# Kernel tuning notes

Measured on AMD Instinct MI355X. Metric: run time of the kernel, lower is better.

## Reference

```python
import jax, jax.numpy as jnp
import numpy as np

B, MN, GN, ME, GE = 1, 40962, 65160, 327660, 163848
MEMB = EEMB = 256
H1, H2 = 512, 64
EPS = 1e-5


def setup_inputs() -> dict:
    key = jax.random.key(0)
    ks = jax.random.split(key, 16)
    s = 0.05
    return {
        "gx": jax.random.normal(ks[0], (B, GN, MEMB), jnp.float32),
        "mx": jax.random.normal(ks[1], (B, MN, MEMB), jnp.float32),
        "me_i": jax.random.randint(ks[2], (2, ME), 0, MN),
        "me_x": jax.random.normal(ks[3], (B, ME, EEMB), jnp.float32),
        "g2me_i": jax.random.randint(ks[4], (2, GE), 0, MN),
        "g2me_x": jax.random.normal(ks[5], (B, GE, EEMB), jnp.float32),
        "m2ge_i": jax.random.randint(ks[6], (2, GE), 0, MN),
        "m2ge_x": jax.random.normal(ks[7], (B, GE, EEMB), jnp.float32),
        # learned params (Linear stored as [in, out]; y = x @ W + b, math-equivalent to torch)
        "W1": jax.random.normal(ks[8], (2 * MEMB + EEMB, H1), jnp.float32) * s,
        "b1": jnp.zeros((H1,), jnp.float32),
        "W2": jax.random.normal(ks[9], (H1, H2), jnp.float32) * s,
        "b2": jnp.zeros((H2,), jnp.float32),
        "W3": jax.random.normal(ks[10], (H2, EEMB), jnp.float32) * s,
        "b3": jnp.zeros((EEMB,), jnp.float32),
        # LayerNorm([m_enum, eemb]) -> elementwise affine over last two dims
        "ln_w": jnp.ones((ME, EEMB), jnp.float32),
        "ln_b": jnp.zeros((ME, EEMB), jnp.float32),
    }


def reference(gx, mx, me_i, me_x, g2me_i, g2me_x, m2ge_i, m2ge_x,
              W1, b1, W2, b2, W3, b3, ln_w, ln_b):
    row, col = me_i[0], me_i[1]
    # gather sender/receiver mesh-node features per edge: [B, ME, 2*MEMB+EEMB]
    h = jnp.concatenate([mx[:, row], mx[:, col], me_x], axis=-1)
    h = jax.nn.silu(h @ W1 + b1)
    h = jax.nn.silu(h @ W2 + b2)
    h = h @ W3 + b3
    # LayerNorm over the last TWO dims (m_enum, eemb), as nn.LayerNorm([m_enum, eemb])
    mean = jnp.mean(h, axis=(-2, -1), keepdims=True)
    var = jnp.var(h, axis=(-2, -1), keepdims=True)
    h = (h - mean) * jax.lax.rsqrt(var + EPS) * ln_w + ln_b
    me_x_new = me_x + h
    return (gx, mx, me_i, me_x_new, g2me_i, g2me_x, m2ge_i, m2ge_x)
```

## Files before the change

### kernel.cpp

```cpp
#include <hip/hip_runtime.h>
#include <hip/hip_bf16.h>

typedef unsigned short u16;
typedef unsigned int u32;
typedef __attribute__((ext_vector_type(8))) short bfrag8;
typedef __attribute__((ext_vector_type(4))) float f32x4;

#define ME_N 327660
#define MN_N 40962
#define MEMB_N 256
#define H1_N 512
#define H2_N 64
#define EEMB_N 256
#define LN_EPS 1e-5f
#define NBLK 5120

static __device__ __forceinline__ u16 f2bf(float f) {
  __hip_bfloat16 h = __float2bfloat16(f);
  return *reinterpret_cast<u16*>(&h);
}
static __device__ __forceinline__ float bf2f(u16 u) {
  union { u32 i; float f; } x; x.i = ((u32)u) << 16; return x.f;
}
static __device__ __forceinline__ u32 pack2(float a, float b) {
  return (u32)f2bf(a) | ((u32)f2bf(b) << 16);
}
static __device__ __forceinline__ float silu_f(float x) {
  return x / (1.0f + __expf(-x));
}
static __device__ __forceinline__ void gload_lds16(const void* g, void* l) {
  __builtin_amdgcn_global_load_lds(
      (const __attribute__((address_space(1))) void*)g,
      (__attribute__((address_space(3))) void*)l, 16, 0, 0);
}

__global__ void i2f_kernel(const int* __restrict__ src, float* __restrict__ dst, int n) {
  int i = blockIdx.x * 256 + threadIdx.x;
  if (i < n) dst[i] = (float)src[i];
}

__global__ void bfconv_kernel(const float* __restrict__ src, u16* __restrict__ dst, int n) {
  int i = (blockIdx.x * 256 + threadIdx.x) * 8;
  if (i >= n) return;
  float4 v0 = reinterpret_cast<const float4*>(src + i)[0];
  float4 v1 = reinterpret_cast<const float4*>(src + i)[1];
  uint4 q;
  q.x = pack2(v0.x, v0.y); q.y = pack2(v0.z, v0.w);
  q.z = pack2(v1.x, v1.y); q.w = pack2(v1.z, v1.w);
  *reinterpret_cast<uint4*>(dst + i) = q;
}

__global__ void wconv1_kernel(const float* __restrict__ src, u16* __restrict__ dst) {
  int i = blockIdx.x * 256 + threadIdx.x;
  if (i >= 512 * 768) return;
  int e   = i & 7;
  int l16 = (i >> 3) & 15;
  int k4  = (i >> 7) & 3;
  int ks  = (i >> 9) & 1;
  int rest = i >> 10;
  int kc = rest % 12;
  int J  = rest / 12;
  int n = J * 16 + l16;
  int k = kc * 64 + ks * 32 + k4 * 8 + e;
  dst[i] = f2bf(src[(size_t)k * 512 + n]);
}

__global__ void wconv_kernel(const float* __restrict__ src, u16* __restrict__ dst,
                             int K, int N) {
  int i = blockIdx.x * 256 + threadIdx.x;
  if (i >= K * N) return;
  int n = i / K;
  int k = i - n * K;
  dst[i] = f2bf(src[(size_t)k * N + n]);
}

__launch_bounds__(256, 2)
__global__ void gemm_fused_kernel(const u16* __restrict__ mxb, const int* __restrict__ me_i,
                                  const float* __restrict__ me_x,
                                  const u16* __restrict__ w1f, const float* __restrict__ b1,
                                  const u16* __restrict__ w2t, const float* __restrict__ b2,
                                  const u16* __restrict__ w3t, const float* __restrict__ b3,
                                  u16* __restrict__ h3, float* __restrict__ partials) {
  __shared__ u16 S[64 * 520 + 64 * 72];
  __shared__ float red[8];
  u16* Abuf = S;
  u16* h1T  = S;
  u16* h2T  = S + 64 * 520;

  const int t = threadIdx.x;
  const int m0 = blockIdx.x * 64;
  const int lane = t & 63;
  const int wid = t >> 6;
  const int l16 = lane & 15;
  const int k4 = lane >> 4;

  const int c0 = wid * 128 + lane;
  const int c1 = c0 + 64;
  const int r0 = c0 >> 3, r1 = c1 >> 3;
  const int e0s = ((c0 & 7) ^ (r0 & 7)) * 8;
  const int e1s = ((c1 & 7) ^ (r1 & 7)) * 8;
  const int mg0 = min(m0 + r0, ME_N - 1);
  const int mg1 = min(m0 + r1, ME_N - 1);
  const u16* row0r = mxb + (size_t)me_i[mg0] * MEMB_N;
  const u16* row0c = mxb + (size_t)me_i[ME_N + mg0] * MEMB_N;
  const u16* row1r = mxb + (size_t)me_i[mg1] * MEMB_N;
  const u16* row1c = mxb + (size_t)me_i[ME_N + mg1] * MEMB_N;
  const int rr = t >> 2, g = t & 3;
  const float* pe = me_x + (size_t)min(m0 + rr, ME_N - 1) * EEMB_N;
  const int E0 = (g * 16) ^ ((rr & 7) * 8);
  const int E1 = (g * 16 + 8) ^ ((rr & 7) * 8);

  const f32x4 zero = {0.f, 0.f, 0.f, 0.f};
  f32x4 acc[4][8];
#pragma unroll
  for (int i = 0; i < 4; ++i)
#pragma unroll
    for (int j = 0; j < 8; ++j) acc[i][j] = zero;

  auto stage_A = [&](int kcn) {
    if (kcn < 8) {
      const u16* s0 = (kcn < 4 ? row0r : row0c) + ((kcn & 3) * 64 + e0s);
      const u16* s1 = (kcn < 4 ? row1r : row1c) + ((kcn & 3) * 64 + e1s);
      u16* lb = Abuf + (kcn & 1) * 4096 + wid * 1024;
      gload_lds16(s0, lb);
      gload_lds16(s1, lb + 512);
    } else {
      const float4* p4 = reinterpret_cast<const float4*>(pe + (kcn - 8) * 64 + g * 16);
      float4 v0 = p4[0], v1 = p4[1], v2 = p4[2], v3 = p4[3];
      uint4 qa, qb;
      qa.x = pack2(v0.x, v0.y); qa.y = pack2(v0.z, v0.w);
      qa.z = pack2(v1.x, v1.y); qa.w = pack2(v1.z, v1.w);
      qb.x = pack2(v2.x, v2.y); qb.y = pack2(v2.z, v2.w);
      qb.z = pack2(v3.x, v3.y); qb.w = pack2(v3.z, v3.w);
      u16* d = Abuf + (kcn & 1) * 4096 + rr * 64;
      *reinterpret_cast<uint4*>(d + E0) = qa;
      *reinterpret_cast<uint4*>(d + E1) = qb;
    }
  };

  stage_A(0);
  __syncthreads();

  for (int kc = 0; kc < 12; ++kc) {
    if (kc < 11) stage_A(kc + 1);
    bfrag8 bfr[2][8];
    {
      const u16* bb = w1f + (size_t)kc * 1024 + k4 * 128 + l16 * 8;
      const size_t woff = (size_t)(wid * 8) * 12288;
#pragma unroll
      for (int ks = 0; ks < 2; ++ks)
#pragma unroll
        for (int j = 0; j < 8; ++j)
          bfr[ks][j] = *reinterpret_cast<const bfrag8*>(bb + woff + (size_t)j * 12288 + ks * 512);
    }
    const u16* ab = Abuf + (kc & 1) * 4096;
#pragma unroll
    for (int ks = 0; ks < 2; ++ks) {
      bfrag8 a[4];
#pragma unroll
      for (int i = 0; i < 4; ++i)
        a[i] = *reinterpret_cast<const bfrag8*>(
            &ab[(i * 16 + l16) * 64 + ((ks * 32 + k4 * 8) ^ ((l16 & 7) * 8))]);
#pragma unroll
      for (int i = 0; i < 4; ++i)
#pragma unroll
        for (int j = 0; j < 8; ++j)
          acc[i][j] = __builtin_amdgcn_mfma_f32_16x16x32_bf16(a[i], bfr[ks][j], acc[i][j], 0, 0, 0);
    }
    __syncthreads();
  }

  float b1v[8];
#pragma unroll
  for (int j = 0; j < 8; ++j) b1v[j] = b1[wid * 128 + j * 16 + l16];
#pragma unroll
  for (int i = 0; i < 4; ++i)
#pragma unroll
    for (int j = 0; j < 8; ++j)
#pragma unroll
      for (int rg = 0; rg < 4; ++rg) {
        float v = silu_f(acc[i][j][rg] + b1v[j]);
        h1T[(i * 16 + k4 * 4 + rg) * 520 + wid * 128 + j * 16 + l16] = f2bf(v);
      }
  __syncthreads();

  const int n2 = wid * 16 + l16;
  bfrag8 w2f[16];
#pragma unroll
  for (int ks = 0; ks < 16; ++ks)
    w2f[ks] = *reinterpret_cast<const bfrag8*>(w2t + (size_t)n2 * 512 + ks * 32 + k4 * 8);
  f32x4 acc2[4];
#pragma unroll
  for (int i = 0; i < 4; ++i) acc2[i] = zero;
#pragma unroll
  for (int ks = 0; ks < 16; ++ks) {
#pragma unroll
    for (int i = 0; i < 4; ++i) {
      bfrag8 a2 = *reinterpret_cast<const bfrag8*>(&h1T[(i * 16 + l16) * 520 + ks * 32 + k4 * 8]);
      acc2[i] = __builtin_amdgcn_mfma_f32_16x16x32_bf16(a2, w2f[ks], acc2[i], 0, 0, 0);
    }
  }
  const float b2v = b2[n2];
#pragma unroll
  for (int i = 0; i < 4; ++i)
#pragma unroll
    for (int rg = 0; rg < 4; ++rg) {
      float v = silu_f(acc2[i][rg] + b2v);
      h2T[(i * 16 + k4 * 4 + rg) * 72 + n2] = f2bf(v);
    }
  __syncthreads();

  bfrag8 w3f[4][2];
#pragma unroll
  for (int j = 0; j < 4; ++j)
#pragma unroll
    for (int ks = 0; ks < 2; ++ks)
      w3f[j][ks] = *reinterpret_cast<const bfrag8*>(
          w3t + (size_t)(wid * 64 + j * 16 + l16) * 64 + ks * 32 + k4 * 8);
  f32x4 acc3[4][4];
#pragma unroll
  for (int i = 0; i < 4; ++i)
#pragma unroll
    for (int j = 0; j < 4; ++j) acc3[i][j] = zero;
#pragma unroll
  for (int ks = 0; ks < 2; ++ks) {
    bfrag8 a3[4];
#pragma unroll
    for (int i = 0; i < 4; ++i)
      a3[i] = *reinterpret_cast<const bfrag8*>(&h2T[(i * 16 + l16) * 72 + ks * 32 + k4 * 8]);
#pragma unroll
    for (int i = 0; i < 4; ++i)
#pragma unroll
      for (int j = 0; j < 4; ++j)
        acc3[i][j] = __builtin_amdgcn_mfma_f32_16x16x32_bf16(a3[i], w3f[j][ks], acc3[i][j], 0, 0, 0);
  }

  float b3v[4];
#pragma unroll
  for (int j = 0; j < 4; ++j) b3v[j] = b3[wid * 64 + j * 16 + l16];
  float lsum = 0.f, lsq = 0.f;
#pragma unroll
  for (int i = 0; i < 4; ++i)
#pragma unroll
    for (int rg = 0; rg < 4; ++rg) {
      int m = m0 + i * 16 + k4 * 4 + rg;
      if (m < ME_N) {
#pragma unroll
        for (int j = 0; j < 4; ++j) {
          float v = acc3[i][j][rg] + b3v[j];
          h3[(size_t)m * EEMB_N + wid * 64 + j * 16 + l16] = f2bf(v);
          lsum += v;
          lsq += v * v;
        }
      }
    }
#pragma unroll
  for (int o = 32; o > 0; o >>= 1) {
    lsum += __shfl_down(lsum, o, 64);
    lsq  += __shfl_down(lsq, o, 64);
  }
  if (lane == 0) { red[wid] = lsum; red[4 + wid] = lsq; }
  __syncthreads();
  if (t == 0) {
    partials[2 * blockIdx.x]     = red[0] + red[1] + red[2] + red[3];
    partials[2 * blockIdx.x + 1] = red[4] + red[5] + red[6] + red[7];
  }
}

__global__ void reduce_kernel(const float* __restrict__ partials, int n,
                              float* __restrict__ stats) {
  __shared__ float s1[256], s2[256];
  float a = 0.f, b = 0.f;
  for (int i = threadIdx.x; i < n; i += 256) { a += partials[2 * i]; b += partials[2 * i + 1]; }
  s1[threadIdx.x] = a; s2[threadIdx.x] = b;
  __syncthreads();
  for (int off = 128; off > 0; off >>= 1) {
    if ((int)threadIdx.x < off) {
      s1[threadIdx.x] += s1[threadIdx.x + off];
      s2[threadIdx.x] += s2[threadIdx.x + off];
    }
    __syncthreads();
  }
  if (threadIdx.x == 0) {
    double cnt = (double)ME_N * (double)EEMB_N;
    double mean = (double)s1[0] / cnt;
    double var = (double)s2[0] / cnt - mean * mean;
    stats[0] = (float)mean;
    stats[1] = (float)(1.0 / sqrt(var + (double)LN_EPS));
  }
}

__launch_bounds__(256)
__global__ void final_kernel(const u16* __restrict__ h3, const float* __restrict__ me_x,
                             const float* __restrict__ ln_w, const float* __restrict__ ln_b,
                             const float* __restrict__ stats, float* __restrict__ out) {
  const size_t total = (size_t)ME_N * EEMB_N;
  size_t i = ((size_t)blockIdx.x * 256 + threadIdx.x) * 8;
  if (i >= total) return;
  const float mean = stats[0], inv = stats[1];
  uint4 hv = *reinterpret_cast<const uint4*>(h3 + i);
  float h[8];
  h[0] = bf2f((u16)(hv.x & 0xffff)); h[1] = bf2f((u16)(hv.x >> 16));
  h[2] = bf2f((u16)(hv.y & 0xffff)); h[3] = bf2f((u16)(hv.y >> 16));
  h[4] = bf2f((u16)(hv.z & 0xffff)); h[5] = bf2f((u16)(hv.z >> 16));
  h[6] = bf2f((u16)(hv.w & 0xffff)); h[7] = bf2f((u16)(hv.w >> 16));
  float4 m0 = reinterpret_cast<const float4*>(me_x + i)[0];
  float4 m1 = reinterpret_cast<const float4*>(me_x + i)[1];
  float4 w0 = reinterpret_cast<const float4*>(ln_w + i)[0];
  float4 w1 = reinterpret_cast<const float4*>(ln_w + i)[1];
  float4 c0 = reinterpret_cast<const float4*>(ln_b + i)[0];
  float4 c1 = reinterpret_cast<const float4*>(ln_b + i)[1];
  float4 o0, o1;
  o0.x = m0.x + (h[0] - mean) * inv * w0.x + c0.x;
  o0.y = m0.y + (h[1] - mean) * inv * w0.y + c0.y;
  o0.z = m0.z + (h[2] - mean) * inv * w0.z + c0.z;
  o0.w = m0.w + (h[3] - mean) * inv * w0.w + c0.w;
  o1.x = m1.x + (h[4] - mean) * inv * w1.x + c1.x;
  o1.y = m1.y + (h[5] - mean) * inv * w1.y + c1.y;
  o1.z = m1.z + (h[6] - mean) * inv * w1.z + c1.z;
  o1.w = m1.w + (h[7] - mean) * inv * w1.w + c1.w;
  reinterpret_cast<float4*>(out + i)[0] = o0;
  reinterpret_cast<float4*>(out + i)[1] = o1;
}

extern "C" void kernel_launch(void* const* d_in, const int* in_sizes, int n_in,
                              void* d_out, int out_size, void* d_ws, size_t ws_size,
                              hipStream_t stream) {
  const float* mx   = (const float*)d_in[1];
  const int*   me_i = (const int*)d_in[2];
  const float* me_x = (const float*)d_in[3];
  const float* W1 = (const float*)d_in[8];
  const float* b1 = (const float*)d_in[9];
  const float* W2 = (const float*)d_in[10];
  const float* b2 = (const float*)d_in[11];
  const float* W3 = (const float*)d_in[12];
  const float* b3 = (const float*)d_in[13];
  const float* ln_w = (const float*)d_in[14];
  const float* ln_b = (const float*)d_in[15];

  char* ws = (char*)d_ws;
  u16* w1f = (u16*)(ws + 0);
  u16* w2t = (u16*)(ws + 786432);
  u16* w3t = (u16*)(ws + 851968);
  u16* mxb = (u16*)(ws + 884736);
  u16* h3  = (u16*)(ws + 21857280);
  float* partials = (float*)(ws + 189619200);
  float* stats    = (float*)(ws + 189660160);

  size_t off[8]; size_t a = 0;
  for (int i = 0; i < 8; ++i) { off[i] = a; a += (size_t)in_sizes[i]; }

  for (int i = 0; i < 8; ++i) {
    if (i == 3) continue;
    if (i == 2 || i == 4 || i == 6) {
      int n = in_sizes[i];
      i2f_kernel<<<(n + 255) / 256, 256, 0, stream>>>(
          (const int*)d_in[i], (float*)d_out + off[i], n);
    } else {
      hipMemcpyAsync((char*)d_out + off[i] * 4, d_in[i], (size_t)in_sizes[i] * 4,
                     hipMemcpyDeviceToDevice, stream);
    }
  }

  wconv1_kernel<<<(512 * 768 + 255) / 256, 256, 0, stream>>>(W1, w1f);
  wconv_kernel<<<(512 * 64 + 255) / 256, 256, 0, stream>>>(W2, w2t, 512, 64);
  wconv_kernel<<<(64 * 256 + 255) / 256, 256, 0, stream>>>(W3, w3t, 64, 256);
  {
    int n = MN_N * MEMB_N;
    bfconv_kernel<<<(n / 8 + 255) / 256, 256, 0, stream>>>(mx, mxb, n);
  }

  gemm_fused_kernel<<<NBLK, 256, 0, stream>>>(mxb, me_i, me_x, w1f, b1, w2t, b2,
                                              w3t, b3, h3, partials);
  reduce_kernel<<<1, 256, 0, stream>>>(partials, NBLK, stats);

  const size_t total8 = (size_t)ME_N * EEMB_N / 8;
  final_kernel<<<(int)((total8 + 255) / 256), 256, 0, stream>>>(
      h3, me_x, ln_w, ln_b, stats, (float*)d_out + off[3]);
}
```

Measured before the change: 911.8 us.

## Rework fused MLP kernel to 8 waves with smaller LDS and coalesced output

Moves the fused edge-MLP kernel from 4 to 8 waves per 64-row block and shrinks shared memory from about 75KB to 32KB, so more blocks and waves can be resident per CU. Layer 1 switches MFMA operand order, so each wave holds a 16-row by 64-column slice of the output instead of 32 registers' worth of accumulator tiles. Layer 2 is split-K across wave halves, with each half computing its own h1 half and the partial sums reduced through LDS. Layer 3 results are staged in swizzled LDS and written to h3 as coalesced 16-byte rows; the workspace offsets shift so the padded last block can write past the real row count. This adds extra barriers and an LDS reduction step, and lowers the per-thread register budget, which risks spills.

```diff
diff --git a/kernel.cpp b/kernel.cpp
--- a/kernel.cpp
+++ b/kernel.cpp
@@ -74,67 +74,51 @@
   dst[i] = f2bf(src[(size_t)k * N + n]);
 }
 
-__launch_bounds__(256, 2)
+__launch_bounds__(512, 4)
 __global__ void gemm_fused_kernel(const u16* __restrict__ mxb, const int* __restrict__ me_i,
                                   const float* __restrict__ me_x,
                                   const u16* __restrict__ w1f, const float* __restrict__ b1,
                                   const u16* __restrict__ w2t, const float* __restrict__ b2,
                                   const u16* __restrict__ w3t, const float* __restrict__ b3,
                                   u16* __restrict__ h3, float* __restrict__ partials) {
-  __shared__ u16 S[64 * 520 + 64 * 72];
-  __shared__ float red[8];
-  u16* Abuf = S;
-  u16* h1T  = S;
-  u16* h2T  = S + 64 * 520;
+  __shared__ u16 S[16384];
+  __shared__ float red[16];
 
   const int t = threadIdx.x;
   const int m0 = blockIdx.x * 64;
   const int lane = t & 63;
-  const int wid = t >> 6;
+  const int w = t >> 6;
   const int l16 = lane & 15;
   const int k4 = lane >> 4;
-
-  const int c0 = wid * 128 + lane;
-  const int c1 = c0 + 64;
-  const int r0 = c0 >> 3, r1 = c1 >> 3;
-  const int e0s = ((c0 & 7) ^ (r0 & 7)) * 8;
-  const int e1s = ((c1 & 7) ^ (r1 & 7)) * 8;
-  const int mg0 = min(m0 + r0, ME_N - 1);
-  const int mg1 = min(m0 + r1, ME_N - 1);
-  const u16* row0r = mxb + (size_t)me_i[mg0] * MEMB_N;
-  const u16* row0c = mxb + (size_t)me_i[ME_N + mg0] * MEMB_N;
-  const u16* row1r = mxb + (size_t)me_i[mg1] * MEMB_N;
-  const u16* row1c = mxb + (size_t)me_i[ME_N + mg1] * MEMB_N;
-  const int rr = t >> 2, g = t & 3;
-  const float* pe = me_x + (size_t)min(m0 + rr, ME_N - 1) * EEMB_N;
-  const int E0 = (g * 16) ^ ((rr & 7) * 8);
-  const int E1 = (g * 16 + 8) ^ ((rr & 7) * 8);
+  const int h7 = l16 & 7;
+
+  const int r_st = t >> 3;
+  const int g_st = t & 7;
+  const int gsw = ((g_st ^ (r_st & 7)) * 8);
+  const int mg = min(m0 + r_st, ME_N - 1);
+  const u16* rowr = mxb + (size_t)me_i[mg] * MEMB_N;
+  const u16* rowc = mxb + (size_t)me_i[ME_N + mg] * MEMB_N;
+  const float* pe = me_x + (size_t)mg * EEMB_N;
 
   const f32x4 zero = {0.f, 0.f, 0.f, 0.f};
-  f32x4 acc[4][8];
-#pragma unroll
-  for (int i = 0; i < 4; ++i)
-#pragma unroll
-    for (int j = 0; j < 8; ++j) acc[i][j] = zero;
+  f32x4 acc[4][4];
+#pragma unroll
+  for (int jj = 0; jj < 4; ++jj)
+#pragma unroll
+    for (int i = 0; i < 4; ++i) acc[jj][i] = zero;
 
   auto stage_A = [&](int kcn) {
+    const int buf = (kcn & 1) * 4096;
     if (kcn < 8) {
-      const u16* s0 = (kcn < 4 ? row0r : row0c) + ((kcn & 3) * 64 + e0s);
-      const u16* s1 = (kcn < 4 ? row1r : row1c) + ((kcn & 3) * 64 + e1s);
-      u16* lb = Abuf + (kcn & 1) * 4096 + wid * 1024;
-      gload_lds16(s0, lb);
-      gload_lds16(s1, lb + 512);
+      const u16* src = (kcn < 4 ? rowr : rowc) + (kcn & 3) * 64 + gsw;
+      gload_lds16(src, S + buf + w * 512);
     } else {
-      const float4* p4 = reinterpret_cast<const float4*>(pe + (kcn - 8) * 64 + g * 16);
-      float4 v0 = p4[0], v1 = p4[1], v2 = p4[2], v3 = p4[3];
-      uint4 qa, qb;
-      qa.x = pack2(v0.x, v0.y); qa.y = pack2(v0.z, v0.w);
-      qa.z = pack2(v1.x, v1.y); qa.w = pack2(v1.z, v1.w);
-      qb.x = pack2(v2.x, v2.y); qb.y = pack2(v2.z, v2.w);
-      qb.z = pack2(v3.x, v3.y); qb.w = pack2(v3.z, v3.w);
-      u16* d = Abuf + (kcn & 1) * 4096 + rr * 64;
-      *reinterpret_cast<uint4*>(d + E0) = qa;
-      *reinterpret_cast<uint4*>(d + E1) = qb;
+      const float4* p4 = reinterpret_cast<const float4*>(pe + (kcn - 8) * 64 + g_st * 8);
+      float4 v0 = p4[0], v1 = p4[1];
+      uint4 q;
+      q.x = pack2(v0.x, v0.y); q.y = pack2(v0.z, v0.w);
+      q.z = pack2(v1.x, v1.y); q.w = pack2(v1.z, v1.w);
+      *reinterpret_cast<uint4*>(S + buf + r_st * 64 + gsw) = q;
     }
   };
 
@@ -143,127 +127,169 @@
 
   for (int kc = 0; kc < 12; ++kc) {
     if (kc < 11) stage_A(kc + 1);
-    bfrag8 bfr[2][8];
-    {
-      const u16* bb = w1f + (size_t)kc * 1024 + k4 * 128 + l16 * 8;
-      const size_t woff = (size_t)(wid * 8) * 12288;
-#pragma unroll
-      for (int ks = 0; ks < 2; ++ks)
-#pragma unroll
-        for (int j = 0; j < 8; ++j)
-          bfr[ks][j] = *reinterpret_cast<const bfrag8*>(bb + woff + (size_t)j * 12288 + ks * 512);
-    }
-    const u16* ab = Abuf + (kc & 1) * 4096;
+    const u16* ab = S + (kc & 1) * 4096;
+    const u16* wb = w1f + (size_t)w * 12288 + (size_t)kc * 1024 + k4 * 128 + l16 * 8;
 #pragma unroll
     for (int ks = 0; ks < 2; ++ks) {
       bfrag8 a[4];
 #pragma unroll
       for (int i = 0; i < 4; ++i)
         a[i] = *reinterpret_cast<const bfrag8*>(
-            &ab[(i * 16 + l16) * 64 + ((ks * 32 + k4 * 8) ^ ((l16 & 7) * 8))]);
-#pragma unroll
-      for (int i = 0; i < 4; ++i)
-#pragma unroll
-        for (int j = 0; j < 8; ++j)
-          acc[i][j] = __builtin_amdgcn_mfma_f32_16x16x32_bf16(a[i], bfr[ks][j], acc[i][j], 0, 0, 0);
+            &ab[(i * 16 + l16) * 64 + (((ks * 4 + k4) ^ h7) * 8)]);
+#pragma unroll
+      for (int jj = 0; jj < 4; ++jj) {
+        bfrag8 bf = *reinterpret_cast<const bfrag8*>(wb + (size_t)jj * 98304 + ks * 512);
+#pragma unroll
+        for (int i = 0; i < 4; ++i)
+          acc[jj][i] = __builtin_amdgcn_mfma_f32_16x16x32_bf16(bf, a[i], acc[jj][i], 0, 0, 0);
+      }
     }
     __syncthreads();
   }
 
-  float b1v[8];
-#pragma unroll
-  for (int j = 0; j < 8; ++j) b1v[j] = b1[wid * 128 + j * 16 + l16];
-#pragma unroll
-  for (int i = 0; i < 4; ++i)
-#pragma unroll
-    for (int j = 0; j < 8; ++j)
-#pragma unroll
-      for (int rg = 0; rg < 4; ++rg) {
-        float v = silu_f(acc[i][j][rg] + b1v[j]);
-        h1T[(i * 16 + k4 * 4 + rg) * 520 + wid * 128 + j * 16 + l16] = f2bf(v);
+  const int kh = w >> 2;
+  const int g4 = w & 3;
+  const int n2 = g4 * 16 + l16;
+  bfrag8 w2f8[8];
+#pragma unroll
+  for (int ksl = 0; ksl < 8; ++ksl)
+    w2f8[ksl] = *reinterpret_cast<const bfrag8*>(
+        w2t + (size_t)n2 * 512 + kh * 256 + ksl * 32 + k4 * 8);
+
+  f32x4 acc2p[4];
+#pragma unroll
+  for (int i = 0; i < 4; ++i) acc2p[i] = zero;
+
+#pragma unroll
+  for (int h = 0; h < 2; ++h) {
+#pragma unroll
+    for (int jr = 0; jr < 2; ++jr) {
+      const int jj = 2 * h + jr;
+      const float4 bq = *reinterpret_cast<const float4*>(b1 + jj * 128 + w * 16 + k4 * 4);
+      const int col = jr * 128 + w * 16 + k4 * 4;
+      const int grp = col >> 3, off = col & 7;
+#pragma unroll
+      for (int i = 0; i < 4; ++i) {
+        float x0 = silu_f(acc[jj][i][0] + bq.x);
+        float x1 = silu_f(acc[jj][i][1] + bq.y);
+        float x2 = silu_f(acc[jj][i][2] + bq.z);
+        float x3 = silu_f(acc[jj][i][3] + bq.w);
+        uint2 pq = make_uint2(pack2(x0, x1), pack2(x2, x3));
+        *reinterpret_cast<uint2*>(&S[(i * 16 + l16) * 256 + ((grp ^ h7) * 8 + off)]) = pq;
       }
-  __syncthreads();
-
-  const int n2 = wid * 16 + l16;
-  bfrag8 w2f[16];
-#pragma unroll
-  for (int ks = 0; ks < 16; ++ks)
-    w2f[ks] = *reinterpret_cast<const bfrag8*>(w2t + (size_t)n2 * 512 + ks * 32 + k4 * 8);
-  f32x4 acc2[4];
-#pragma unroll
-  for (int i = 0; i < 4; ++i) acc2[i] = zero;
-#pragma unroll
-  for (int ks = 0; ks < 16; ++ks) {
+    }
+    __syncthreads();
+    if (kh == h) {
+#pragma unroll
+      for (int ksl = 0; ksl < 8; ++ksl) {
+#pragma unroll
+        for (int i = 0; i < 4; ++i) {
+          bfrag8 a2 = *reinterpret_cast<const bfrag8*>(
+              &S[(i * 16 + l16) * 256 + (((ksl * 4 + k4) ^ h7) * 8)]);
+          acc2p[i] = __builtin_amdgcn_mfma_f32_16x16x32_bf16(w2f8[ksl], a2, acc2p[i], 0, 0, 0);
+        }
+      }
+    }
+    __syncthreads();
+  }
+
+  float* LDSf = reinterpret_cast<float*>(S);
+  u16* h2T = S + 12288;
+  if (kh == 1) {
+#pragma unroll
+    for (int i = 0; i < 4; ++i)
+      *reinterpret_cast<f32x4*>(&LDSf[((g4 * 4 + i) * 64 + lane) * 4]) = acc2p[i];
+  }
+  __syncthreads();
+  if (kh == 0) {
+    const float4 b2q = *reinterpret_cast<const float4*>(b2 + g4 * 16 + k4 * 4);
+    const int col = g4 * 16 + k4 * 4;
+    const int grp = col >> 3, off = col & 7;
 #pragma unroll
     for (int i = 0; i < 4; ++i) {
-      bfrag8 a2 = *reinterpret_cast<const bfrag8*>(&h1T[(i * 16 + l16) * 520 + ks * 32 + k4 * 8]);
-      acc2[i] = __builtin_amdgcn_mfma_f32_16x16x32_bf16(a2, w2f[ks], acc2[i], 0, 0, 0);
-    }
-  }
-  const float b2v = b2[n2];
-#pragma unroll
-  for (int i = 0; i < 4; ++i)
-#pragma unroll
-    for (int rg = 0; rg < 4; ++rg) {
-      float v = silu_f(acc2[i][rg] + b2v);
-      h2T[(i * 16 + k4 * 4 + rg) * 72 + n2] = f2bf(v);
-    }
-  __syncthreads();
-
-  bfrag8 w3f[4][2];
-#pragma unroll
-  for (int j = 0; j < 4; ++j)
+      f32x4 o = *reinterpret_cast<f32x4*>(&LDSf[((g4 * 4 + i) * 64 + lane) * 4]);
+      float x0 = silu_f(acc2p[i][0] + o[0] + b2q.x);
+      float x1 = silu_f(acc2p[i][1] + o[1] + b2q.y);
+      float x2 = silu_f(acc2p[i][2] + o[2] + b2q.z);
+      float x3 = silu_f(acc2p[i][3] + o[3] + b2q.w);
+      uint2 pq = make_uint2(pack2(x0, x1), pack2(x2, x3));
+      *reinterpret_cast<uint2*>(&h2T[(i * 16 + l16) * 64 + ((grp ^ h7) * 8 + off)]) = pq;
+    }
+  }
+  __syncthreads();
+
+  bfrag8 a3[2][4];
+#pragma unroll
+  for (int ks = 0; ks < 2; ++ks)
+#pragma unroll
+    for (int i = 0; i < 4; ++i)
+      a3[ks][i] = *reinterpret_cast<const bfrag8*>(
+          &h2T[(i * 16 + l16) * 64 + (((ks * 4 + k4) ^ h7) * 8)]);
+  bfrag8 w3f[2][2];
+#pragma unroll
+  for (int j = 0; j < 2; ++j)
 #pragma unroll
     for (int ks = 0; ks < 2; ++ks)
       w3f[j][ks] = *reinterpret_cast<const bfrag8*>(
-          w3t + (size_t)(wid * 64 + j * 16 + l16) * 64 + ks * 32 + k4 * 8);
-  f32x4 acc3[4][4];
-#pragma unroll
-  for (int i = 0; i < 4; ++i)
-#pragma unroll
-    for (int j = 0; j < 4; ++j) acc3[i][j] = zero;
-#pragma unroll
-  for (int ks = 0; ks < 2; ++ks) {
-    bfrag8 a3[4];
-#pragma unroll
-    for (int i = 0; i < 4; ++i)
-      a3[i] = *reinterpret_cast<const bfrag8*>(&h2T[(i * 16 + l16) * 72 + ks * 32 + k4 * 8]);
-#pragma unroll
-    for (int i = 0; i < 4; ++i)
-#pragma unroll
-      for (int j = 0; j < 4; ++j)
-        acc3[i][j] = __builtin_amdgcn_mfma_f32_16x16x32_bf16(a3[i], w3f[j][ks], acc3[i][j], 0, 0, 0);
-  }
-
-  float b3v[4];
-#pragma unroll
-  for (int j = 0; j < 4; ++j) b3v[j] = b3[wid * 64 + j * 16 + l16];
+          w3t + (size_t)(w * 32 + j * 16 + l16) * 64 + ks * 32 + k4 * 8);
+  __syncthreads();
+
+  f32x4 acc3[2][4];
+#pragma unroll
+  for (int j = 0; j < 2; ++j)
+#pragma unroll
+    for (int i = 0; i < 4; ++i) acc3[j][i] = zero;
+#pragma unroll
+  for (int ks = 0; ks < 2; ++ks)
+#pragma unroll
+    for (int j = 0; j < 2; ++j)
+#pragma unroll
+      for (int i = 0; i < 4; ++i)
+        acc3[j][i] = __builtin_amdgcn_mfma_f32_16x16x32_bf16(w3f[j][ks], a3[ks][i], acc3[j][i], 0, 0, 0);
+
   float lsum = 0.f, lsq = 0.f;
 #pragma unroll
-  for (int i = 0; i < 4; ++i)
-#pragma unroll
-    for (int rg = 0; rg < 4; ++rg) {
-      int m = m0 + i * 16 + k4 * 4 + rg;
-      if (m < ME_N) {
-#pragma unroll
-        for (int j = 0; j < 4; ++j) {
-          float v = acc3[i][j][rg] + b3v[j];
-          h3[(size_t)m * EEMB_N + wid * 64 + j * 16 + l16] = f2bf(v);
-          lsum += v;
-          lsq += v * v;
-        }
+  for (int j = 0; j < 2; ++j) {
+    const float4 b3q = *reinterpret_cast<const float4*>(b3 + w * 32 + j * 16 + k4 * 4);
+    const int col = w * 32 + j * 16 + k4 * 4;
+    const int grp = col >> 3, off = col & 7;
+#pragma unroll
+    for (int i = 0; i < 4; ++i) {
+      float x0 = acc3[j][i][0] + b3q.x;
+      float x1 = acc3[j][i][1] + b3q.y;
+      float x2 = acc3[j][i][2] + b3q.z;
+      float x3 = acc3[j][i][3] + b3q.w;
+      if (m0 + i * 16 + l16 < ME_N) {
+        lsum += (x0 + x1) + (x2 + x3);
+        lsq += x0 * x0 + x1 * x1 + x2 * x2 + x3 * x3;
       }
-    }
+      uint2 pq = make_uint2(pack2(x0, x1), pack2(x2, x3));
+      *reinterpret_cast<uint2*>(&S[(i * 16 + l16) * 256 + ((grp ^ h7) * 8 + off)]) = pq;
+    }
+  }
 #pragma unroll
   for (int o = 32; o > 0; o >>= 1) {
     lsum += __shfl_down(lsum, o, 64);
     lsq  += __shfl_down(lsq, o, 64);
   }
-  if (lane == 0) { red[wid] = lsum; red[4 + wid] = lsq; }
-  __syncthreads();
+  if (lane == 0) { red[w] = lsum; red[8 + w] = lsq; }
+  __syncthreads();
+
+  {
+    u16* dst = h3 + (size_t)(m0 + r_st) * EEMB_N;
+#pragma unroll
+    for (int q = 0; q < 4; ++q) {
+      const int G = q * 8 + g_st;
+      uint4 v = *reinterpret_cast<const uint4*>(&S[r_st * 256 + ((G ^ (r_st & 7)) * 8)]);
+      *reinterpret_cast<uint4*>(dst + G * 8) = v;
+    }
+  }
   if (t == 0) {
-    partials[2 * blockIdx.x]     = red[0] + red[1] + red[2] + red[3];
-    partials[2 * blockIdx.x + 1] = red[4] + red[5] + red[6] + red[7];
+    float s1 = 0.f, s2 = 0.f;
+#pragma unroll
+    for (int q = 0; q < 8; ++q) { s1 += red[q]; s2 += red[8 + q]; }
+    partials[2 * blockIdx.x] = s1;
+    partials[2 * blockIdx.x + 1] = s2;
   }
 }
 
@@ -344,8 +370,8 @@
   u16* w3t = (u16*)(ws + 851968);
   u16* mxb = (u16*)(ws + 884736);
   u16* h3  = (u16*)(ws + 21857280);
-  float* partials = (float*)(ws + 189619200);
-  float* stats    = (float*)(ws + 189660160);
+  float* partials = (float*)(ws + 189629440);
+  float* stats    = (float*)(ws + 189670400);
 
   size_t off[8]; size_t a = 0;
   for (int i = 0; i < 8; ++i) { off[i] = a; a += (size_t)in_sizes[i]; }
@@ -370,7 +396,7 @@
     bfconv_kernel<<<(n / 8 + 255) / 256, 256, 0, stream>>>(mx, mxb, n);
   }
 
-  gemm_fused_kernel<<<NBLK, 256, 0, stream>>>(mxb, me_i, me_x, w1f, b1, w2t, b2,
+  gemm_fused_kernel<<<NBLK, 512, 0, stream>>>(mxb, me_i, me_x, w1f, b1, w2t, b2,
                                               w3t, b3, h3, partials);
   reduce_kernel<<<1, 256, 0, stream>>>(partials, NBLK, stats);
 
```

Result: no change. 915.5 us (+0.4%).
